# Performance work log

Hardware: AMD Instinct MI355X
Metric: run time of the kernel (lower is better)

The kernel has to match this reference:

```python
import jax, jax.numpy as jnp
import numpy as np

DIM_MODEL = 1024
DIM_K = 1024
DIM_V = 1024


def setup_inputs() -> dict:
    key = jax.random.key(0)
    ks = jax.random.split(key, 7)
    B, S = 4, 2048
    scale = 1.0 / np.sqrt(DIM_MODEL)
    return {
        "x": jax.random.normal(ks[0], (B, S, DIM_MODEL), dtype=jnp.float32),
        # weights stored [in, out] (transpose of torch Linear.weight)
        "Wq": jax.random.normal(ks[1], (DIM_MODEL, DIM_K), dtype=jnp.float32) * scale,
        "Wk": jax.random.normal(ks[2], (DIM_MODEL, DIM_K), dtype=jnp.float32) * scale,
        "Wv": jax.random.normal(ks[3], (DIM_MODEL, DIM_V), dtype=jnp.float32) * scale,
        "Wo": jax.random.normal(ks[4], (DIM_V, DIM_MODEL), dtype=jnp.float32) * (1.0 / np.sqrt(DIM_V)),
        "ln2_gamma": jnp.ones((DIM_MODEL,), dtype=jnp.float32),
        "ln2_beta": jnp.zeros((DIM_MODEL,), dtype=jnp.float32),
    }


def _layernorm(x, gamma, beta, eps=1e-5):
    mu = jnp.mean(x, axis=-1, keepdims=True)
    var = jnp.var(x, axis=-1, keepdims=True)
    return (x - mu) * jax.lax.rsqrt(var + eps) * gamma + beta


def reference(x, Wq, Wk, Wv, Wo, ln2_gamma, ln2_beta):
    # single-head attention, x: [B,S,D]
    q = jnp.einsum("bsd,dk->bsk", x, Wq)
    k = jnp.einsum("bsd,dk->bsk", x, Wk)
    v = jnp.einsum("bsd,dv->bsv", x, Wv)
    scores = jnp.einsum("bqk,bsk->bqs", q, k) / jnp.sqrt(jnp.asarray(DIM_K, x.dtype))
    attn = jax.nn.softmax(scores, axis=-1)  # [B,S,S]
    ctx = jnp.einsum("bqs,bsv->bqv", attn, v)
    hidden = jnp.einsum("bqv,vd->bqd", ctx, Wo)
    hidden = _layernorm(hidden, ln2_gamma, ln2_beta)
    return hidden
```

## Files before the change

### kernel.cpp

```cpp
#include <hip/hip_runtime.h>
#include <hip/hip_bf16.h>
#include <stdint.h>

typedef __bf16 bf16;
typedef __attribute__((ext_vector_type(8))) __bf16 bf16x8;
typedef __attribute__((ext_vector_type(4))) __bf16 bf16x4;
typedef __attribute__((ext_vector_type(4))) float f32x4;

#define AS1 __attribute__((address_space(1)))
#define AS3 __attribute__((address_space(3)))

__device__ __forceinline__ void gl_lds16(const void* g, void* l) {
  __builtin_amdgcn_global_load_lds((const AS1 uint32_t*)g, (AS3 uint32_t*)l, 16, 0, 0);
}

template <int MODE>
__global__ __launch_bounds__(256) void gemm128(
    const bf16* __restrict__ Abase, const bf16* __restrict__ Bbase,
    bf16* __restrict__ Cbase, int K, int lda, int ldb, int ldc,
    long long sA, long long sB, long long sC, float alpha,
    float* __restrict__ lsum, bf16* __restrict__ C2, bf16* __restrict__ C3) {
  extern __shared__ char smem[];
  const int z = blockIdx.z;
  const bf16* A = Abase + (long long)z * sA;
  const bf16* B = Bbase + (long long)z * sB;
  bf16* C = Cbase + (long long)z * sC;
  const int m0 = blockIdx.y * 128, n0 = blockIdx.x * 128;
  const int t = threadIdx.x;
  const int lane = t & 63, wave = t >> 6;
  const int wm = (wave >> 1) * 64, wn = (wave & 1) * 64;
  const int quad = lane >> 4, r = lane & 15;

  const int srow = t >> 3;
  const int schunk = (t & 7) ^ (srow & 7);
  const bf16* ga = A + (long long)(m0 + srow) * lda + schunk * 8;
  const bf16* gb = B + (long long)(n0 + srow) * ldb + schunk * 8;
  char* la = smem + t * 16;
  char* lb = smem + 16384 + t * 16;

  f32x4 acc[4][4] = {};

  for (int k0 = 0; k0 < K; k0 += 64) {
    __syncthreads();
#pragma unroll
    for (int rd = 0; rd < 4; rd++) {
      gl_lds16(ga + (long long)(32 * rd) * lda, la + rd * 4096);
      gl_lds16(gb + (long long)(32 * rd) * ldb, lb + rd * 4096);
    }
    ga += 64;
    gb += 64;
    __syncthreads();

#pragma unroll
    for (int kk = 0; kk < 2; kk++) {
      bf16x8 af[4], bfr[4];
      const int csa = ((kk * 4 + quad) ^ (r & 7)) * 16;
      const char* pa = smem + (wm + r) * 128 + csa;
      const char* pb = smem + 16384 + (wn + r) * 128 + csa;
#pragma unroll
      for (int i = 0; i < 4; i++) af[i] = *(const bf16x8*)(pa + i * 2048);
#pragma unroll
      for (int j = 0; j < 4; j++) bfr[j] = *(const bf16x8*)(pb + j * 2048);
#pragma unroll
      for (int i = 0; i < 4; i++)
#pragma unroll
        for (int j = 0; j < 4; j++)
          acc[i][j] = __builtin_amdgcn_mfma_f32_16x16x32_bf16(af[i], bfr[j],
                                                              acc[i][j], 0, 0, 0);
    }
  }

  if constexpr (MODE == 4) {
    bf16* dst;
    int c0;
    if (n0 < 1024) {
      dst = Cbase; c0 = n0;
    } else if (n0 < 2048) {
      dst = C2; c0 = n0 - 1024;
    } else {
      dst = C3; c0 = n0 - 2048;
    }
#pragma unroll
    for (int i = 0; i < 4; i++) {
      const int row0 = m0 + wm + i * 16 + quad * 4;
#pragma unroll
      for (int j = 0; j < 4; j++) {
        const int col = c0 + wn + j * 16 + r;
#pragma unroll
        for (int rg = 0; rg < 4; rg++)
          dst[(long long)(row0 + rg) * 1024 + col] = (bf16)acc[i][j][rg];
      }
    }
    return;
  }

#pragma unroll
  for (int i = 0; i < 4; i++) {
    const int row0 = m0 + wm + i * 16 + quad * 4;
    float rsum[4] = {0.f, 0.f, 0.f, 0.f};
    float inv[4];
    if constexpr (MODE == 2) {
#pragma unroll
      for (int rg = 0; rg < 4; rg++)
        inv[rg] = 1.f / lsum[(long long)z * 2048 + row0 + rg];
    }
#pragma unroll
    for (int j = 0; j < 4; j++) {
      const int col = n0 + wn + j * 16 + r;
#pragma unroll
      for (int rg = 0; rg < 4; rg++) {
        float v = acc[i][j][rg] * alpha;
        if constexpr (MODE == 1) {
          bf16 eb = (bf16)__expf(v);
          C[(long long)(row0 + rg) * ldc + col] = eb;
          rsum[rg] += (float)eb;
        } else if constexpr (MODE == 2) {
          C[(long long)(row0 + rg) * ldc + col] = (bf16)(v * inv[rg]);
        } else {
          C[(long long)(row0 + rg) * ldc + col] = (bf16)v;
        }
      }
    }
    if constexpr (MODE == 1) {
#pragma unroll
      for (int rg = 0; rg < 4; rg++) {
#pragma unroll
        for (int off = 8; off >= 1; off >>= 1)
          rsum[rg] += __shfl_xor(rsum[rg], off);
        if (r == 0)
          atomicAdd(&lsum[(long long)z * 2048 + row0 + rg], rsum[rg]);
      }
    }
  }
}

__global__ __launch_bounds__(256) void prep(
    const float* __restrict__ x, const float* __restrict__ Wq,
    const float* __restrict__ Wk, const float* __restrict__ Wv,
    const float* __restrict__ Wo, bf16* __restrict__ Xb,
    bf16* __restrict__ Wcat, bf16* __restrict__ Wot,
    float* __restrict__ lsum) {
  __shared__ float tile[32][33];
  const int bx = blockIdx.x;
  const int t = threadIdx.x;
  if (bx < 4096) {
    if (bx < 32) lsum[bx * 256 + t] = 0.f;
    long long i = (long long)bx * 256 + t;
    const float4* p = (const float4*)x;
    float4 a = p[i * 2], b = p[i * 2 + 1];
    bf16x8 o;
    o[0] = (bf16)a.x; o[1] = (bf16)a.y; o[2] = (bf16)a.z; o[3] = (bf16)a.w;
    o[4] = (bf16)b.x; o[5] = (bf16)b.y; o[6] = (bf16)b.z; o[7] = (bf16)b.w;
    ((bf16x8*)Xb)[i] = o;
  } else {
    int idx = bx - 4096;
    const int zw = idx >> 10;
    idx &= 1023;
    const int tiy = idx >> 5, tix = idx & 31;
    const float* W = (zw == 0) ? Wq : (zw == 1) ? Wk : (zw == 2) ? Wv : Wo;
    bf16* dst = (zw < 3) ? (Wcat + (long long)zw * 1024 * 1024) : Wot;
    const int bx0 = tix * 32, by0 = tiy * 32;
    const int ttx = t & 31, tty = t >> 5;
#pragma unroll
    for (int i = 0; i < 32; i += 8)
      tile[tty + i][ttx] = W[(long long)(by0 + tty + i) * 1024 + bx0 + ttx];
    __syncthreads();
#pragma unroll
    for (int i = 0; i < 32; i += 8)
      dst[(long long)(bx0 + tty + i) * 1024 + by0 + ttx] = (bf16)tile[ttx][tty + i];
  }
}

__global__ __launch_bounds__(256) void layernorm_rows(
    const bf16* __restrict__ H, const float* __restrict__ gamma,
    const float* __restrict__ beta, float* __restrict__ O) {
  const long long row = blockIdx.x;
  const bf16* h = H + row * 1024;
  float* o = O + row * 1024;
  const int t = threadIdx.x;
  const int lane = t & 63, wave = t >> 6;
  bf16x4 hv = ((const bf16x4*)h)[t];
  float v[4] = {(float)hv[0], (float)hv[1], (float)hv[2], (float)hv[3]};
  float s = v[0] + v[1] + v[2] + v[3];
  float ss = v[0] * v[0] + v[1] * v[1] + v[2] * v[2] + v[3] * v[3];
#pragma unroll
  for (int off = 32; off >= 1; off >>= 1) {
    s += __shfl_xor(s, off);
    ss += __shfl_xor(ss, off);
  }
  __shared__ float rs[4], rss[4];
  if (lane == 0) {
    rs[wave] = s;
    rss[wave] = ss;
  }
  __syncthreads();
  s = rs[0] + rs[1] + rs[2] + rs[3];
  ss = rss[0] + rss[1] + rss[2] + rss[3];
  const float mean = s * (1.f / 1024.f);
  const float var = ss * (1.f / 1024.f) - mean * mean;
  const float rstd = rsqrtf(var + 1e-5f);
  float4 g = ((const float4*)gamma)[t];
  float4 bb = ((const float4*)beta)[t];
  float4 rr;
  rr.x = (v[0] - mean) * rstd * g.x + bb.x;
  rr.y = (v[1] - mean) * rstd * g.y + bb.y;
  rr.z = (v[2] - mean) * rstd * g.z + bb.z;
  rr.w = (v[3] - mean) * rstd * g.w + bb.w;
  ((float4*)o)[t] = rr;
}

extern "C" void kernel_launch(void* const* d_in, const int* in_sizes, int n_in,
                              void* d_out, int out_size, void* d_ws,
                              size_t ws_size, hipStream_t stream) {
  const float* x = (const float*)d_in[0];
  const float* Wq = (const float*)d_in[1];
  const float* Wk = (const float*)d_in[2];
  const float* Wv = (const float*)d_in[3];
  const float* Wo = (const float*)d_in[4];
  const float* gamma = (const float*)d_in[5];
  const float* beta = (const float*)d_in[6];
  float* out = (float*)d_out;

  char* ws = (char*)d_ws;
  const size_t MB = 1024ull * 1024ull;
  bf16* Xb = (bf16*)(ws + 0);
  bf16* Wcat = (bf16*)(ws + 16 * MB);
  bf16* Wot = (bf16*)(ws + 22 * MB);
  bf16* Qd = (bf16*)(ws + 24 * MB);
  bf16* Kd = (bf16*)(ws + 40 * MB);
  bf16* Vd = (bf16*)(ws + 56 * MB);
  bf16* expS = (bf16*)(ws + 72 * MB);
  float* lsum = (float*)(ws + 104 * MB);
  bf16* VWo = (bf16*)(ws + 105 * MB);
  bf16* Hd = (bf16*)(ws + 121 * MB);

  prep<<<8192, 256, 0, stream>>>(x, Wq, Wk, Wv, Wo, Xb, Wcat, Wot, lsum);

  gemm128<4><<<dim3(24, 64, 1), 256, 32768, stream>>>(
      Xb, Wcat, Qd, 1024, 1024, 1024, 1024, 0, 0, 0, 1.f, nullptr, Kd, Vd);

  gemm128<1><<<dim3(16, 16, 4), 256, 32768, stream>>>(
      Qd, Kd, expS, 1024, 1024, 1024, 2048, 2048 * 1024LL, 2048 * 1024LL,
      2048 * 2048LL, 0.03125f, lsum, nullptr, nullptr);

  gemm128<0><<<dim3(16, 8, 4), 256, 32768, stream>>>(
      Wot, Vd, VWo, 1024, 1024, 1024, 2048, 0, 2048 * 1024LL, 1024 * 2048LL,
      1.f, nullptr, nullptr, nullptr);

  gemm128<2><<<dim3(8, 16, 4), 256, 32768, stream>>>(
      expS, VWo, Hd, 2048, 2048, 2048, 1024, 2048 * 2048LL, 1024 * 2048LL,
      2048 * 1024LL, 1.f, lsum, nullptr, nullptr);

  layernorm_rows<<<8192, 256, 0, stream>>>(Hd, gamma, beta, out);
}
```

Baseline: 282.5 us.

## Add 256x256 double-buffered pipelined GEMM kernel for QKV, scores and output GEMMs

Adds a 512-thread GEMM kernel with 256x256 tiles and two 64 KB LDS buffers. It interleaves global-to-LDS loads for the next K-step with MFMA work on the current one, using split barriers, vmcnt waits and setprio. The QKV, exp-scores and PV GEMMs now use it, while the Wo·V GEMM stays on the old 128-tile kernel, which is trimmed to plain store mode. The goal is to cut LDS/global traffic per FLOP and hide load latency, at the cost of fewer blocks (128-384 per launch) and heavy register and LDS use that may limit occupancy.

New measurement: 279.8 us. About the same (-1.0%).

```diff
diff --git a/kernel.cpp b/kernel.cpp
--- a/kernel.cpp
+++ b/kernel.cpp
@@ -12,6 +12,210 @@
 
 __device__ __forceinline__ void gl_lds16(const void* g, void* l) {
   __builtin_amdgcn_global_load_lds((const AS1 uint32_t*)g, (AS3 uint32_t*)l, 16, 0, 0);
+}
+
+#define FENCE() asm volatile("" ::: "memory")
+#define BAR()                        \
+  do {                               \
+    FENCE();                         \
+    __builtin_amdgcn_s_barrier();    \
+    FENCE();                         \
+  } while (0)
+#define VMW4() asm volatile("s_waitcnt vmcnt(4)" ::: "memory")
+
+template <int MODE>
+__global__ __launch_bounds__(512, 2) void gemm256(
+    const bf16* __restrict__ Abase, const bf16* __restrict__ Bbase,
+    bf16* __restrict__ Cbase, int K, int lda, int ldb, int ldc,
+    long long sA, long long sB, long long sC, float alpha,
+    float* __restrict__ lsum, bf16* __restrict__ C2, bf16* __restrict__ C3) {
+  extern __shared__ char smem[];
+  const int z = blockIdx.z;
+  const bf16* A = Abase + (long long)z * sA;
+  const bf16* B = Bbase + (long long)z * sB;
+  bf16* C = Cbase + (long long)z * sC;
+  const int m0 = blockIdx.y * 256, n0 = blockIdx.x * 256;
+  const int t = threadIdx.x;
+  const int lane = t & 63;
+  const int wid = t >> 6, wrow = wid >> 2, wcol = wid & 3;
+  const int quad = lane >> 4, r = lane & 15;
+
+  const int rowq = t >> 3;
+  const int chunk = (t & 7) ^ (rowq & 7);
+  const bf16* pA0 = A + (long long)(m0 + rowq) * lda + chunk * 8;
+  const bf16* pB0 = B + (long long)(n0 + rowq) * ldb + chunk * 8;
+
+  const int aoff = (wrow * 64 + r) * 128;
+  const int boff = 32768 + (wcol * 32 + r) * 128;
+  const int cs0 = ((quad) ^ (r & 7)) * 16;
+  const int cs1 = ((4 + quad) ^ (r & 7)) * 16;
+
+#define STAGE_A(HALF, KT, SB)                                                  \
+  do {                                                                         \
+    gl_lds16(pA0 + (long long)((HALF) * 128) * lda + (KT),                     \
+             (SB) + (HALF) * 16384 + t * 16);                                  \
+    gl_lds16(pA0 + (long long)((HALF) * 128 + 64) * lda + (KT),                \
+             (SB) + (HALF) * 16384 + 8192 + t * 16);                           \
+  } while (0)
+#define STAGE_B(HALF, KT, SB)                                                  \
+  do {                                                                         \
+    gl_lds16(pB0 + (long long)((HALF) * 128) * ldb + (KT),                     \
+             (SB) + 32768 + (HALF) * 16384 + t * 16);                          \
+    gl_lds16(pB0 + (long long)((HALF) * 128 + 64) * ldb + (KT),                \
+             (SB) + 32768 + (HALF) * 16384 + 8192 + t * 16);                   \
+  } while (0)
+#define READ_A(MH)                                                             \
+  _Pragma("unroll") for (int mr = 0; mr < 4; ++mr) {                           \
+    af[mr][0] = *(const bf16x8*)(Sc + (MH) * 16384 + aoff + mr * 2048 + cs0);  \
+    af[mr][1] = *(const bf16x8*)(Sc + (MH) * 16384 + aoff + mr * 2048 + cs1);  \
+  }
+#define READ_B(NH)                                                             \
+  _Pragma("unroll") for (int nr = 0; nr < 2; ++nr) {                           \
+    bfr[NH][nr][0] =                                                           \
+        *(const bf16x8*)(Sc + (NH) * 16384 + boff + nr * 2048 + cs0);          \
+    bfr[NH][nr][1] =                                                           \
+        *(const bf16x8*)(Sc + (NH) * 16384 + boff + nr * 2048 + cs1);          \
+  }
+#define MMA(MH, NH)                                                            \
+  _Pragma("unroll") for (int mr = 0; mr < 4; ++mr)                             \
+      _Pragma("unroll") for (int nr = 0; nr < 2; ++nr) {                       \
+    acc[MH][NH][mr][nr] = __builtin_amdgcn_mfma_f32_16x16x32_bf16(             \
+        af[mr][0], bfr[NH][nr][0], acc[MH][NH][mr][nr], 0, 0, 0);              \
+    acc[MH][NH][mr][nr] = __builtin_amdgcn_mfma_f32_16x16x32_bf16(             \
+        af[mr][1], bfr[NH][nr][1], acc[MH][NH][mr][nr], 0, 0, 0);              \
+  }
+
+  f32x4 acc[2][2][4][2] = {};
+  bf16x8 af[4][2];
+  bf16x8 bfr[2][2][2];
+  char* Sc = smem;
+  char* Sn = smem + 65536;
+  const int T = K >> 6;
+
+  STAGE_A(0, 0, Sc);
+  STAGE_B(0, 0, Sc);
+  STAGE_A(1, 0, Sc);
+  STAGE_B(1, 0, Sc);
+  {
+    const int kt1p = (T > 1) ? 64 : 0;
+    STAGE_A(0, kt1p, Sn);
+    STAGE_B(0, kt1p, Sn);
+  }
+  VMW4();
+  BAR();
+
+  for (int tt = 0; tt < T; ++tt) {
+    const int kt1 = (tt + 1 < T ? tt + 1 : 0) << 6;
+    const int kt2 = (tt + 2 < T ? tt + 2 : 0) << 6;
+    READ_A(0);
+    READ_B(0);
+    STAGE_A(1, kt1, Sn);
+    __builtin_amdgcn_s_setprio(1);
+    MMA(0, 0);
+    __builtin_amdgcn_s_setprio(0);
+    BAR();
+    READ_B(1);
+    STAGE_B(1, kt1, Sn);
+    __builtin_amdgcn_s_setprio(1);
+    MMA(0, 1);
+    __builtin_amdgcn_s_setprio(0);
+    BAR();
+    READ_A(1);
+    STAGE_A(0, kt2, Sc);
+    __builtin_amdgcn_s_setprio(1);
+    MMA(1, 0);
+    __builtin_amdgcn_s_setprio(0);
+    BAR();
+    STAGE_B(0, kt2, Sc);
+    __builtin_amdgcn_s_setprio(1);
+    MMA(1, 1);
+    __builtin_amdgcn_s_setprio(0);
+    VMW4();
+    BAR();
+    char* tp = Sc;
+    Sc = Sn;
+    Sn = tp;
+  }
+
+  if constexpr (MODE == 4) {
+    bf16* dst;
+    int c0;
+    if (n0 < 1024) {
+      dst = Cbase;
+      c0 = n0;
+    } else if (n0 < 2048) {
+      dst = C2;
+      c0 = n0 - 1024;
+    } else {
+      dst = C3;
+      c0 = n0 - 2048;
+    }
+#pragma unroll
+    for (int mh = 0; mh < 2; ++mh)
+#pragma unroll
+      for (int mr = 0; mr < 4; ++mr) {
+        const int row0 = m0 + mh * 128 + wrow * 64 + mr * 16 + quad * 4;
+#pragma unroll
+        for (int nh = 0; nh < 2; ++nh)
+#pragma unroll
+          for (int nr = 0; nr < 2; ++nr) {
+            const int col = c0 + nh * 128 + wcol * 32 + nr * 16 + r;
+#pragma unroll
+            for (int rg = 0; rg < 4; ++rg)
+              dst[(long long)(row0 + rg) * 1024 + col] =
+                  (bf16)acc[mh][nh][mr][nr][rg];
+          }
+      }
+    return;
+  }
+
+#pragma unroll
+  for (int mh = 0; mh < 2; ++mh)
+#pragma unroll
+    for (int mr = 0; mr < 4; ++mr) {
+      const int row0 = m0 + mh * 128 + wrow * 64 + mr * 16 + quad * 4;
+      float rsum[4] = {0.f, 0.f, 0.f, 0.f};
+      float inv[4];
+      if constexpr (MODE == 2) {
+#pragma unroll
+        for (int rg = 0; rg < 4; ++rg)
+          inv[rg] = 1.f / lsum[(long long)z * 2048 + row0 + rg];
+      }
+#pragma unroll
+      for (int nh = 0; nh < 2; ++nh)
+#pragma unroll
+        for (int nr = 0; nr < 2; ++nr) {
+          const int col = n0 + nh * 128 + wcol * 32 + nr * 16 + r;
+#pragma unroll
+          for (int rg = 0; rg < 4; ++rg) {
+            float v = acc[mh][nh][mr][nr][rg] * alpha;
+            if constexpr (MODE == 1) {
+              bf16 eb = (bf16)__expf(v);
+              C[(long long)(row0 + rg) * ldc + col] = eb;
+              rsum[rg] += (float)eb;
+            } else if constexpr (MODE == 2) {
+              C[(long long)(row0 + rg) * ldc + col] = (bf16)(v * inv[rg]);
+            } else {
+              C[(long long)(row0 + rg) * ldc + col] = (bf16)v;
+            }
+          }
+        }
+      if constexpr (MODE == 1) {
+#pragma unroll
+        for (int rg = 0; rg < 4; ++rg) {
+#pragma unroll
+          for (int off = 8; off >= 1; off >>= 1)
+            rsum[rg] += __shfl_xor(rsum[rg], off);
+          if (r == 0)
+            atomicAdd(&lsum[(long long)z * 2048 + row0 + rg], rsum[rg]);
+        }
+      }
+    }
+#undef STAGE_A
+#undef STAGE_B
+#undef READ_A
+#undef READ_B
+#undef MMA
 }
 
 template <int MODE>
@@ -70,65 +274,16 @@
     }
   }
 
-  if constexpr (MODE == 4) {
-    bf16* dst;
-    int c0;
-    if (n0 < 1024) {
-      dst = Cbase; c0 = n0;
-    } else if (n0 < 2048) {
-      dst = C2; c0 = n0 - 1024;
-    } else {
-      dst = C3; c0 = n0 - 2048;
-    }
-#pragma unroll
-    for (int i = 0; i < 4; i++) {
-      const int row0 = m0 + wm + i * 16 + quad * 4;
-#pragma unroll
-      for (int j = 0; j < 4; j++) {
-        const int col = c0 + wn + j * 16 + r;
-#pragma unroll
-        for (int rg = 0; rg < 4; rg++)
-          dst[(long long)(row0 + rg) * 1024 + col] = (bf16)acc[i][j][rg];
-      }
-    }
-    return;
-  }
-
 #pragma unroll
   for (int i = 0; i < 4; i++) {
     const int row0 = m0 + wm + i * 16 + quad * 4;
-    float rsum[4] = {0.f, 0.f, 0.f, 0.f};
-    float inv[4];
-    if constexpr (MODE == 2) {
-#pragma unroll
-      for (int rg = 0; rg < 4; rg++)
-        inv[rg] = 1.f / lsum[(long long)z * 2048 + row0 + rg];
-    }
 #pragma unroll
     for (int j = 0; j < 4; j++) {
       const int col = n0 + wn + j * 16 + r;
 #pragma unroll
       for (int rg = 0; rg < 4; rg++) {
         float v = acc[i][j][rg] * alpha;
-        if constexpr (MODE == 1) {
-          bf16 eb = (bf16)__expf(v);
-          C[(long long)(row0 + rg) * ldc + col] = eb;
-          rsum[rg] += (float)eb;
-        } else if constexpr (MODE == 2) {
-          C[(long long)(row0 + rg) * ldc + col] = (bf16)(v * inv[rg]);
-        } else {
-          C[(long long)(row0 + rg) * ldc + col] = (bf16)v;
-        }
-      }
-    }
-    if constexpr (MODE == 1) {
-#pragma unroll
-      for (int rg = 0; rg < 4; rg++) {
-#pragma unroll
-        for (int off = 8; off >= 1; off >>= 1)
-          rsum[rg] += __shfl_xor(rsum[rg], off);
-        if (r == 0)
-          atomicAdd(&lsum[(long long)z * 2048 + row0 + rg], rsum[rg]);
+        C[(long long)(row0 + rg) * ldc + col] = (bf16)v;
       }
     }
   }
@@ -234,12 +389,23 @@
   bf16* VWo = (bf16*)(ws + 105 * MB);
   bf16* Hd = (bf16*)(ws + 121 * MB);
 
+  static int inited = 0;
+  if (!inited) {
+    hipFuncSetAttribute(reinterpret_cast<const void*>(&gemm256<4>),
+                        hipFuncAttributeMaxDynamicSharedMemorySize, 131072);
+    hipFuncSetAttribute(reinterpret_cast<const void*>(&gemm256<1>),
+                        hipFuncAttributeMaxDynamicSharedMemorySize, 131072);
+    hipFuncSetAttribute(reinterpret_cast<const void*>(&gemm256<2>),
+                        hipFuncAttributeMaxDynamicSharedMemorySize, 131072);
+    inited = 1;
+  }
+
   prep<<<8192, 256, 0, stream>>>(x, Wq, Wk, Wv, Wo, Xb, Wcat, Wot, lsum);
 
-  gemm128<4><<<dim3(24, 64, 1), 256, 32768, stream>>>(
+  gemm256<4><<<dim3(12, 32, 1), 512, 131072, stream>>>(
       Xb, Wcat, Qd, 1024, 1024, 1024, 1024, 0, 0, 0, 1.f, nullptr, Kd, Vd);
 
-  gemm128<1><<<dim3(16, 16, 4), 256, 32768, stream>>>(
+  gemm256<1><<<dim3(8, 8, 4), 512, 131072, stream>>>(
       Qd, Kd, expS, 1024, 1024, 1024, 2048, 2048 * 1024LL, 2048 * 1024LL,
       2048 * 2048LL, 0.03125f, lsum, nullptr, nullptr);
 
@@ -247,7 +413,7 @@
       Wot, Vd, VWo, 1024, 1024, 1024, 2048, 0, 2048 * 1024LL, 1024 * 2048LL,
       1.f, nullptr, nullptr, nullptr);
 
-  gemm128<2><<<dim3(8, 16, 4), 256, 32768, stream>>>(
+  gemm256<2><<<dim3(4, 8, 4), 512, 131072, stream>>>(
       expS, VWo, Hd, 2048, 2048, 2048, 1024, 2048 * 2048LL, 1024 * 2048LL,
       2048 * 1024LL, 1.f, lsum, nullptr, nullptr);
 
```
